# Performance work log

Measured on AMD Instinct MI355X. Metric: run time of the kernel, lower is better.

## Reference

```python
import jax, jax.numpy as jnp
import numpy as np

BATCH, D, Q = 8192, 256, 16

def setup_inputs() -> dict:
    key = jax.random.key(0)
    X = jax.random.normal(key, (BATCH, D, Q), dtype=jnp.float32)
    return {"X": X}

def reference(X):
    # Re-orthonormalization: thin QR, return the orthonormal factor Q (batch, d, q)
    Qm, _R = jnp.linalg.qr(X, mode="reduced")
    return Qm
```

## Files before the change

### kernel.cpp

```cpp
#include <hip/hip_runtime.h>


constexpr int BATCH = 8192;
constexpr int DROWS = 256;
constexpr int QC    = 16;

typedef _Float16 half8 __attribute__((ext_vector_type(8)));
typedef float    f32x4 __attribute__((ext_vector_type(4)));

__device__ __forceinline__ float rdlane(float v, int l) {
    return __int_as_float(__builtin_amdgcn_readlane(__float_as_int(v), l));
}

template <int CTRL>
__device__ __forceinline__ float dpp_add(float x) {
    int y = __builtin_amdgcn_update_dpp(0, __float_as_int(x), CTRL, 0xf, 0xf, true);
    return x + __int_as_float(y);
}

__device__ __forceinline__ float wave_sum32(float x) {
    x = dpp_add<0xB1>(x);
    x = dpp_add<0x4E>(x);
    x = dpp_add<0x141>(x);
    x = dpp_add<0x140>(x);
    x = dpp_add<0x142>(x);
    return rdlane(x, 31);
}

__device__ __forceinline__ float2 dual_sum32(float x) {
    x = dpp_add<0xB1>(x);
    x = dpp_add<0x4E>(x);
    x = dpp_add<0x141>(x);
    x = dpp_add<0x140>(x);
    x = dpp_add<0x142>(x);
    return make_float2(rdlane(x, 31), rdlane(x, 63));
}

__global__ __launch_bounds__(256) void qr_dual_r8(
    const float* __restrict__ in, float* __restrict__ out)
{
    const int lane = threadIdx.x & 63;
    const int wid  = threadIdx.x >> 6;
    const int b    = blockIdx.x * 4 + wid;

    __shared__ __align__(16) char smem[4][2 * QC * 72 * 2];
    unsigned short* hp = reinterpret_cast<unsigned short*>(smem[wid]);
    unsigned short* lp = hp + QC * 72;

    const float4* __restrict__ A4 = (const float4*)(in  + (size_t)b * (DROWS * QC));
    float4*       __restrict__ O4 = (float4*)      (out + (size_t)b * (DROWS * QC));

    float x[4][QC];

#pragma unroll
    for (int s = 0; s < 4; ++s) {
        const int rr = s * 64 + lane;
#pragma unroll
        for (int q4 = 0; q4 < 4; ++q4) {
            float4 t = A4[rr * 4 + q4];
            x[s][q4*4+0] = t.x; x[s][q4*4+1] = t.y;
            x[s][q4*4+2] = t.z; x[s][q4*4+3] = t.w;
        }
    }

    f32x4 accA = {0.f, 0.f, 0.f, 0.f};
    f32x4 accB = {0.f, 0.f, 0.f, 0.f};
    const int cm   = lane & 15;
    const int g4   = lane >> 4;
    const int fidx = cm * 72 + 8 * g4;

#pragma unroll
    for (int s = 0; s < 4; ++s) {
#pragma unroll
        for (int c = 0; c < QC; ++c) {
            float v = x[s][c];
            if (s == 0) v = (lane < QC) ? 0.f : v;
            _Float16 hh = (_Float16)v;
            float     r = v - (float)hh;
            _Float16 ll = (_Float16)r;
            union { _Float16 f; unsigned short u; } ch, cl;
            ch.f = hh; cl.f = ll;
            hp[c * 72 + lane] = ch.u;
            lp[c * 72 + lane] = cl.u;
        }
        asm volatile("" ::: "memory");
#pragma unroll
        for (int h = 0; h < 2; ++h) {
            const half8 fh = *reinterpret_cast<const half8*>(&hp[fidx + 32 * h]);
            const half8 fl = *reinterpret_cast<const half8*>(&lp[fidx + 32 * h]);
            accA = __builtin_amdgcn_mfma_f32_16x16x32_f16(fh, fh, accA, 0, 0, 0);
            accB = __builtin_amdgcn_mfma_f32_16x16x32_f16(fh, fl, accB, 0, 0, 0);
            accB = __builtin_amdgcn_mfma_f32_16x16x32_f16(fl, fh, accB, 0, 0, 0);
            accA = __builtin_amdgcn_mfma_f32_16x16x32_f16(fl, fl, accA, 0, 0, 0);
        }
        asm volatile("" ::: "memory");
    }
    const f32x4 Gf = accA + accB;

    float* gbuf = reinterpret_cast<float*>(smem[wid]);
    asm volatile("" ::: "memory");
#pragma unroll
    for (int q = 0; q < 4; ++q) gbuf[(4 * g4 + q) * 20 + cm] = Gf[q];
    asm volatile("" ::: "memory");
    float g[QC];
#pragma unroll
    for (int k = 0; k < 4; ++k) {
        const f32x4 t = *reinterpret_cast<const f32x4*>(&gbuf[(lane & 15) * 20 + 4 * k]);
        g[4*k+0] = t[0]; g[4*k+1] = t[1]; g[4*k+2] = t[2]; g[4*k+3] = t[3];
    }

    const int li = lane - 16;

    float rs = 0.f;
#pragma unroll
    for (int k = 0; k < QC; ++k) {
        const float piv = rdlane(g[k], 16 + k);
        const float inv = __builtin_amdgcn_rcpf(piv);
        const float rsk = __builtin_amdgcn_rsqf(piv);
        rs = (li == k) ? rsk : rs;
        const float m = (li > k) ? g[k] * inv : 0.f;
#pragma unroll
        for (int j = k + 1; j < QC; ++j) {
            const float bj = rdlane(g[j], 16 + k);
            g[j] = fmaf(-m, bj, g[j]);
        }
    }

    float c[QC];
#pragma unroll
    for (int t = 0; t < QC; ++t) {
        const float ub = (li <= t && li >= 0) ? g[t] * rs : 0.f;
        c[t] = (lane < QC) ? x[0][t] : ub;
    }
    const int baddr = (lane & 31) << 2;
#pragma unroll
    for (int t = 0; t < QC; ++t)
        c[t] = __int_as_float(__builtin_amdgcn_ds_bpermute(baddr, __float_as_int(c[t])));

    const bool hi  = (lane >= 32);
    const int  row = lane & 31;

    float nrm2[QC];
#pragma unroll
    for (int m = 0; m < QC; m += 2) {
        const float pc = hi ? c[m + 1] : c[m];
        const float2 ss = dual_sum32(pc * pc);
        nrm2[m] = ss.x; nrm2[m + 1] = ss.y;
    }

#pragma unroll
    for (int j = 0; j < QC; ++j) {
        const float piv   = rdlane(c[j], j);
        const float nrm   = sqrtf(nrm2[j]);
        const float alpha = -copysignf(nrm, piv);
        const float vtv   = 2.f * (nrm2[j] - alpha * piv);
        const float beta  = 2.f * __builtin_amdgcn_rcpf(vtv);
        const float v = (row < j) ? 0.f : ((row == j) ? piv - alpha : c[j]);
        int t = j + 1;
#pragma unroll
        for (; t + 1 < QC; t += 2) {
            const float pc = hi ? c[t + 1] : c[t];
            const float2 d = dual_sum32(v * pc);
            const float wb0 = beta * d.x;
            const float wb1 = beta * d.y;
            c[t]     = fmaf(-wb0, v, c[t]);
            c[t + 1] = fmaf(-wb1, v, c[t + 1]);
            const float rv0 = rdlane(c[t], j);
            const float rv1 = rdlane(c[t + 1], j);
            nrm2[t]     = fmaf(-rv0, rv0, nrm2[t]);
            nrm2[t + 1] = fmaf(-rv1, rv1, nrm2[t + 1]);
        }
        if (t < QC) {
            const float d  = wave_sum32(v * c[t]);
            const float wb = beta * d;
            c[t] = fmaf(-wb, v, c[t]);
            const float rv = rdlane(c[t], j);
            nrm2[t] = fmaf(-rv, rv, nrm2[t]);
        }
        c[j] = (row == j) ? alpha : c[j];
    }

#pragma unroll
    for (int k = 0; k < QC; ++k) {
        const float rkk = rdlane(c[k], k);
        const float ikk = __builtin_amdgcn_rcpf(rkk);
        x[0][k] *= ikk; x[1][k] *= ikk; x[2][k] *= ikk; x[3][k] *= ikk;
#pragma unroll
        for (int t = k + 1; t < QC; ++t) {
            const float r = rdlane(c[t], k);
            x[0][t] = fmaf(-r, x[0][k], x[0][t]);
            x[1][t] = fmaf(-r, x[1][k], x[1][t]);
            x[2][t] = fmaf(-r, x[2][k], x[2][t]);
            x[3][t] = fmaf(-r, x[3][k], x[3][t]);
        }
    }

#pragma unroll
    for (int s = 0; s < 4; ++s) {
        const int rr = s * 64 + lane;
#pragma unroll
        for (int q4 = 0; q4 < 4; ++q4) {
            O4[rr * 4 + q4] = make_float4(x[s][q4*4+0], x[s][q4*4+1],
                                          x[s][q4*4+2], x[s][q4*4+3]);
        }
    }
}

extern "C" void kernel_launch(void* const* d_in, const int* in_sizes, int n_in,
                              void* d_out, int out_size, void* d_ws, size_t ws_size,
                              hipStream_t stream) {
    const float* X = (const float*)d_in[0];
    float*       O = (float*)d_out;
    qr_dual_r8<<<BATCH / 4, 256, 0, stream>>>(X, O);
}
```

Before: 243.2 us.

## Split each matrix across two waves sharing LDS Gram computation

Each QR problem is now handled by a 128-thread block of two waves instead of one wave, and each wave holds half the rows. Both waves write fp16 hi/lo splits into shared LDS and each redundantly computes the full Gram matrix via MFMA, with barriers in between. The top 16 rows are passed through LDS so both waves can run the small Cholesky/Householder step redundantly. The aim is to halve register pressure and per-wave load/store and triangular-solve work, raising parallelism, at the cost of block barriers and duplicated small-matrix work.

After: 240.1 us. Within noise of the previous version (-1.3%).

```diff
diff --git a/kernel.cpp b/kernel.cpp
--- a/kernel.cpp
+++ b/kernel.cpp
@@ -4,6 +4,7 @@
 constexpr int BATCH = 8192;
 constexpr int DROWS = 256;
 constexpr int QC    = 16;
+constexpr int PITCH = 136;
 
 typedef _Float16 half8 __attribute__((ext_vector_type(8)));
 typedef float    f32x4 __attribute__((ext_vector_type(4)));
@@ -36,25 +37,26 @@
     return make_float2(rdlane(x, 31), rdlane(x, 63));
 }
 
-__global__ __launch_bounds__(256) void qr_dual_r8(
+__global__ __launch_bounds__(128) void qr_pair_r11(
     const float* __restrict__ in, float* __restrict__ out)
 {
     const int lane = threadIdx.x & 63;
-    const int wid  = threadIdx.x >> 6;
-    const int b    = blockIdx.x * 4 + wid;
-
-    __shared__ __align__(16) char smem[4][2 * QC * 72 * 2];
-    unsigned short* hp = reinterpret_cast<unsigned short*>(smem[wid]);
-    unsigned short* lp = hp + QC * 72;
+    const int w    = threadIdx.x >> 6;
+    const int b    = blockIdx.x;
+
+    __shared__ __align__(16) char smem[QC * PITCH * 2 * 2 + QC * 20 * 4];
+    unsigned short* hp   = reinterpret_cast<unsigned short*>(smem);
+    unsigned short* lp   = hp + QC * PITCH;
+    float*          gbuf = reinterpret_cast<float*>(smem);
+    float*          xbuf = reinterpret_cast<float*>(smem + QC * PITCH * 2 * 2);
 
     const float4* __restrict__ A4 = (const float4*)(in  + (size_t)b * (DROWS * QC));
     float4*       __restrict__ O4 = (float4*)      (out + (size_t)b * (DROWS * QC));
 
-    float x[4][QC];
-
-#pragma unroll
-    for (int s = 0; s < 4; ++s) {
-        const int rr = s * 64 + lane;
+    float x[2][QC];
+#pragma unroll
+    for (int s = 0; s < 2; ++s) {
+        const int rr = (2 * s + w) * 64 + lane;
 #pragma unroll
         for (int q4 = 0; q4 < 4; ++q4) {
             float4 t = A4[rr * 4 + q4];
@@ -65,39 +67,42 @@
 
     f32x4 accA = {0.f, 0.f, 0.f, 0.f};
     f32x4 accB = {0.f, 0.f, 0.f, 0.f};
-    const int cm   = lane & 15;
-    const int g4   = lane >> 4;
-    const int fidx = cm * 72 + 8 * g4;
-
-#pragma unroll
-    for (int s = 0; s < 4; ++s) {
+    const int cm = lane & 15;
+    const int g4 = lane >> 4;
+
+#pragma unroll
+    for (int t = 0; t < 2; ++t) {
 #pragma unroll
         for (int c = 0; c < QC; ++c) {
-            float v = x[s][c];
-            if (s == 0) v = (lane < QC) ? 0.f : v;
+            float v = x[t][c];
+            if (t == 0 && w == 0) v = (lane < QC) ? 0.f : v;
             _Float16 hh = (_Float16)v;
             float     r = v - (float)hh;
             _Float16 ll = (_Float16)r;
             union { _Float16 f; unsigned short u; } ch, cl;
             ch.f = hh; cl.f = ll;
-            hp[c * 72 + lane] = ch.u;
-            lp[c * 72 + lane] = cl.u;
-        }
-        asm volatile("" ::: "memory");
-#pragma unroll
-        for (int h = 0; h < 2; ++h) {
-            const half8 fh = *reinterpret_cast<const half8*>(&hp[fidx + 32 * h]);
-            const half8 fl = *reinterpret_cast<const half8*>(&lp[fidx + 32 * h]);
+            hp[c * PITCH + w * 64 + lane] = ch.u;
+            lp[c * PITCH + w * 64 + lane] = cl.u;
+        }
+        if (t == 1 && w == 0 && lane < QC) {
+#pragma unroll
+            for (int c = 0; c < QC; ++c) xbuf[lane * 20 + c] = x[0][c];
+        }
+        __syncthreads();
+#pragma unroll
+        for (int h = 0; h < 4; ++h) {
+            const int fi = cm * PITCH + 32 * h + 8 * g4;
+            const half8 fh = *reinterpret_cast<const half8*>(&hp[fi]);
+            const half8 fl = *reinterpret_cast<const half8*>(&lp[fi]);
             accA = __builtin_amdgcn_mfma_f32_16x16x32_f16(fh, fh, accA, 0, 0, 0);
             accB = __builtin_amdgcn_mfma_f32_16x16x32_f16(fh, fl, accB, 0, 0, 0);
             accB = __builtin_amdgcn_mfma_f32_16x16x32_f16(fl, fh, accB, 0, 0, 0);
             accA = __builtin_amdgcn_mfma_f32_16x16x32_f16(fl, fl, accA, 0, 0, 0);
         }
-        asm volatile("" ::: "memory");
+        __syncthreads();
     }
     const f32x4 Gf = accA + accB;
 
-    float* gbuf = reinterpret_cast<float*>(smem[wid]);
     asm volatile("" ::: "memory");
 #pragma unroll
     for (int q = 0; q < 4; ++q) gbuf[(4 * g4 + q) * 20 + cm] = Gf[q];
@@ -126,11 +131,18 @@
         }
     }
 
+    float xtop[QC];
+#pragma unroll
+    for (int k = 0; k < 4; ++k) {
+        const f32x4 t = *reinterpret_cast<const f32x4*>(&xbuf[(lane & 15) * 20 + 4 * k]);
+        xtop[4*k+0] = t[0]; xtop[4*k+1] = t[1]; xtop[4*k+2] = t[2]; xtop[4*k+3] = t[3];
+    }
+
     float c[QC];
 #pragma unroll
     for (int t = 0; t < QC; ++t) {
         const float ub = (li <= t && li >= 0) ? g[t] * rs : 0.f;
-        c[t] = (lane < QC) ? x[0][t] : ub;
+        c[t] = (lane < QC) ? xtop[t] : ub;
     }
     const int baddr = (lane & 31) << 2;
 #pragma unroll
@@ -184,20 +196,18 @@
     for (int k = 0; k < QC; ++k) {
         const float rkk = rdlane(c[k], k);
         const float ikk = __builtin_amdgcn_rcpf(rkk);
-        x[0][k] *= ikk; x[1][k] *= ikk; x[2][k] *= ikk; x[3][k] *= ikk;
+        x[0][k] *= ikk; x[1][k] *= ikk;
 #pragma unroll
         for (int t = k + 1; t < QC; ++t) {
             const float r = rdlane(c[t], k);
             x[0][t] = fmaf(-r, x[0][k], x[0][t]);
             x[1][t] = fmaf(-r, x[1][k], x[1][t]);
-            x[2][t] = fmaf(-r, x[2][k], x[2][t]);
-            x[3][t] = fmaf(-r, x[3][k], x[3][t]);
-        }
-    }
-
-#pragma unroll
-    for (int s = 0; s < 4; ++s) {
-        const int rr = s * 64 + lane;
+        }
+    }
+
+#pragma unroll
+    for (int s = 0; s < 2; ++s) {
+        const int rr = (2 * s + w) * 64 + lane;
 #pragma unroll
         for (int q4 = 0; q4 < 4; ++q4) {
             O4[rr * 4 + q4] = make_float4(x[s][q4*4+0], x[s][q4*4+1],
@@ -211,5 +221,5 @@
                               hipStream_t stream) {
     const float* X = (const float*)d_in[0];
     float*       O = (float*)d_out;
-    qr_dual_r8<<<BATCH / 4, 256, 0, stream>>>(X, O);
-}
+    qr_pair_r11<<<BATCH, 128, 0, stream>>>(X, O);
+}
```
